# Optimization experiments

Measured on AMD Instinct MI355X. Metric: run time of the kernel, lower is better.

## Reference

```python
import jax, jax.numpy as jnp
import numpy as np

N = 100000      # nodes
E = 1600000     # edges (avg degree 16)
D = 128         # in_feats
C = 40          # n_classes
K = 4           # propagation steps
T = 2.0
DELTA = T / K   # 0.5
EPS = 1e-5      # LayerNorm eps


def setup_inputs() -> dict:
    key = jax.random.key(0)
    k1, k2, k3, k4, k5 = jax.random.split(key, 5)
    feat = jax.random.normal(k1, (N, D), jnp.float32)
    row = jax.random.randint(k2, (E,), 0, N, dtype=jnp.int32)
    col = jax.random.randint(k3, (E,), 0, N, dtype=jnp.int32)
    # fc: Linear(D -> C), xavier-ish scale
    W = jax.random.normal(k4, (C, D), jnp.float32) / np.sqrt(D)
    b = jax.random.normal(k5, (C,), jnp.float32) * 0.01
    # LayerNorm params
    gamma = jnp.ones((C,), jnp.float32)
    beta = jnp.zeros((C,), jnp.float32)
    return {"feat": feat, "row": row, "col": col, "W": W, "b": b,
            "gamma": gamma, "beta": beta}


def reference(feat, row, col, W, b, gamma, beta):
    # degrees of augmented adjacency A + I (row counts + self loop)
    deg = jnp.zeros((N,), feat.dtype).at[row].add(1.0) + 1.0
    dinv = jax.lax.rsqrt(deg)
    w_edge = dinv[row] * dinv[col]     # S[row,col] for off-diagonal entries
    w_self = dinv * dinv               # S[i,i] from the added self loop
    # h <- ((1-delta) I + delta S)^K @ feat, applied iteratively (same math as
    # precomputing the matrix power, but never materializes it)
    h = feat
    for _ in range(K):
        agg = jax.ops.segment_sum(h[col] * w_edge[:, None], row, num_segments=N)
        agg = agg + h * w_self[:, None]
        h = (1.0 - DELTA) * h + DELTA * agg
    # fc
    h = h @ W.T + b                    # [N, C]
    # LayerNorm over last dim
    mu = jnp.mean(h, axis=-1, keepdims=True)
    var = jnp.var(h, axis=-1, keepdims=True)
    h = (h - mu) * jax.lax.rsqrt(var + EPS) * gamma + beta
    return h
```

## Files before the change

kernel.cpp:

```cpp
#include <hip/hip_runtime.h>
#include <hip/hip_fp16.h>

#define N_NODES 100000
#define N_EDGES 1600000
#define D_FEAT  128
#define C_CLS   40
#define LN_EPS  1e-5f

#define RPB   256
#define NBKT  ((N_NODES + RPB - 1) / RPB)
#define BCAP  6144
#define TILE_E 4096
#define EBLK  ((N_EDGES + TILE_E - 1) / TILE_E)
#define NTILES (N_NODES / 16)
#define FCB   ((NTILES + 3) / 4)

#define ZPAD  8
#define QLO   ((N_NODES + ZPAD) * 4)
#define ZBYTES ((size_t)(N_NODES + ZPAD) * 80)

typedef __attribute__((ext_vector_type(8))) _Float16 half8;
typedef __attribute__((ext_vector_type(4))) float floatx4;
typedef __attribute__((ext_vector_type(4))) unsigned uintx4;

__device__ inline float2 h2f2(unsigned v) {
    __half2 h = *(__half2*)&v;
    return __half22float2(h);
}
__device__ inline unsigned f2h2(float x, float y) {
    __half2 h = __floats2half2_rn(x, y);
    return *(unsigned*)&h;
}

__global__ __launch_bounds__(256) void init_k(const float* __restrict__ W,
                                              _Float16* __restrict__ wh,
                                              int* __restrict__ bktsz,
                                              unsigned* __restrict__ z0,
                                              unsigned* __restrict__ z1) {
    int t = threadIdx.x;
    if (blockIdx.x < 20) {
        int i = blockIdx.x * 256 + t;
        if (i < C_CLS * D_FEAT) wh[i] = (_Float16)W[i];
        return;
    }
    for (int i = t; i < NBKT; i += 256) bktsz[i] = 0;
    if (t < 16) {
        z0[(size_t)N_NODES * 16 + t] = 0u;
        z1[(size_t)N_NODES * 16 + t] = 0u;
    }
    if (t < 4) {
        z0[(size_t)QLO * 4 + (size_t)N_NODES * 4 + t] = 0u;
        z1[(size_t)QLO * 4 + (size_t)N_NODES * 4 + t] = 0u;
    }
}

__global__ __launch_bounds__(256) void fcbin_k(const float* __restrict__ feat,
                                               const _Float16* __restrict__ wh,
                                               const int* __restrict__ row,
                                               const int* __restrict__ col,
                                               int* __restrict__ bktsz,
                                               int* __restrict__ csr_tmp,
                                               unsigned* __restrict__ z) {
    __shared__ int hist[NBKT];
    __shared__ int cbase[NBKT];
    __shared__ _Float16 zl[4][16][72];
    int t = threadIdx.x;
    if (blockIdx.x < EBLK) {
        int tile = blockIdx.x * TILE_E;
        for (int i = t; i < NBKT; i += 256) hist[i] = 0;
        __syncthreads();
        int r[16], c[16], pos[16];
        #pragma unroll
        for (int k = 0; k < 16; k++) {
            int e = tile + k * 256 + t;
            if (e < N_EDGES) {
                r[k] = row[e]; c[k] = col[e];
                pos[k] = atomicAdd(&hist[r[k] / RPB], 1);
            } else r[k] = -1;
        }
        __syncthreads();
        for (int i = t; i < NBKT; i += 256) {
            int h = hist[i];
            cbase[i] = h ? atomicAdd(&bktsz[i], h) : 0;
        }
        __syncthreads();
        #pragma unroll
        for (int k = 0; k < 16; k++) {
            if (r[k] >= 0) {
                int b = r[k] / RPB;
                int slot = cbase[b] + pos[k];
                if (slot < BCAP)
                    csr_tmp[b * BCAP + slot] = ((r[k] & (RPB - 1)) << 17) | c[k];
            }
        }
        return;
    }
    int wave = t >> 6, lane = t & 63;
    int m = lane & 15, quad = lane >> 4;
    int tile = (blockIdx.x - EBLK) * 4 + wave;
    bool valid = (tile < NTILES);
    int node0 = tile * 16;

    half8 bfrag[3][4];
    if (valid) {
        const half8* wh8 = (const half8*)wh;
        #pragma unroll
        for (int ct = 0; ct < 3; ct++) {
            int c = ct * 16 + m;
            bool ok = (c < C_CLS);
            #pragma unroll
            for (int ks = 0; ks < 4; ks++) {
                if (ok) {
                    bfrag[ct][ks] = wh8[c * 16 + ks * 4 + quad];
                } else {
                    #pragma unroll
                    for (int j = 0; j < 8; j++) bfrag[ct][ks][j] = (_Float16)0.0f;
                }
            }
        }
    }

    floatx4 acc0 = {0.f,0.f,0.f,0.f}, acc1 = acc0, acc2 = acc0;
    if (valid) {
        #pragma unroll
        for (int ks = 0; ks < 4; ks++) {
            const float4* ap = (const float4*)&feat[(node0 + m) * D_FEAT + ks * 32 + quad * 8];
            float4 a0 = ap[0], a1 = ap[1];
            half8 afrag;
            afrag[0] = (_Float16)a0.x; afrag[1] = (_Float16)a0.y;
            afrag[2] = (_Float16)a0.z; afrag[3] = (_Float16)a0.w;
            afrag[4] = (_Float16)a1.x; afrag[5] = (_Float16)a1.y;
            afrag[6] = (_Float16)a1.z; afrag[7] = (_Float16)a1.w;
            acc0 = __builtin_amdgcn_mfma_f32_16x16x32_f16(afrag, bfrag[0][ks], acc0, 0, 0, 0);
            acc1 = __builtin_amdgcn_mfma_f32_16x16x32_f16(afrag, bfrag[1][ks], acc1, 0, 0, 0);
            acc2 = __builtin_amdgcn_mfma_f32_16x16x32_f16(afrag, bfrag[2][ks], acc2, 0, 0, 0);
        }
    }

    if (valid) {
        #pragma unroll
        for (int r = 0; r < 4; r++) {
            int zrow = quad * 4 + r;
            zl[wave][zrow][m]      = (_Float16)acc0[r];
            zl[wave][zrow][16 + m] = (_Float16)acc1[r];
            zl[wave][zrow][32 + m] = (_Float16)acc2[r];
        }
    }
    __syncthreads();
    if (valid) {
        int zr = lane >> 2, part = lane & 3;
        uint4 lo = ((uint4*)&zl[wave][zr][0])[part];
        ((uint4*)z)[(size_t)(node0 + zr) * 4 + part] = lo;
        if (part == 0) {
            uint4 hi = *(uint4*)&zl[wave][zr][32];
            ((uint4*)z)[QLO + node0 + zr] = hi;
        }
    }
}

__global__ __launch_bounds__(256) void refine_k(const int* __restrict__ csr_tmp,
                                                const int* __restrict__ bktsz,
                                                int2* __restrict__ rowinfo,
                                                float2* __restrict__ rowc,
                                                int* __restrict__ csr_col,
                                                unsigned* __restrict__ z) {
    __shared__ int hist[RPB];
    __shared__ int psc[RPB];
    __shared__ int cur[RPB];
    __shared__ float dl[RPB];
    int b = blockIdx.x, t = threadIdx.x;
    int r0 = b * RPB;
    int nrows = min(RPB, N_NODES - r0);
    hist[t] = 0;
    __syncthreads();
    int cnt = bktsz[b];
    const int* base = csr_tmp + b * BCAP;
    for (int i = t; i < cnt; i += 256)
        atomicAdd(&hist[base[i] >> 17], 1);
    __syncthreads();
    int v = hist[t];
    psc[t] = v;
    __syncthreads();
    for (int off = 1; off < 256; off <<= 1) {
        int x = (t >= off) ? psc[t - off] : 0;
        __syncthreads();
        psc[t] += x;
        __syncthreads();
    }
    int start = b * BCAP + psc[t] - v;
    cur[t] = start;
    float fdeg = (float)v + 1.0f;
    float inv  = 1.0f / fdeg;
    dl[t] = rsqrtf(fdeg);
    if (t < nrows) {
        rowinfo[r0 + t] = make_int2(start, start + v);
        rowc[r0 + t]    = make_float2(0.5f + 0.5f * inv,
                                      0.5f * inv);
    }
    __syncthreads();
    for (int i = t; i < cnt; i += 256) {
        int pk = base[i];
        int lr = pk >> 17;
        int p = atomicAdd(&cur[lr], 1);
        csr_col[p] = pk & 0x1FFFF;
    }
    int totlo = nrows * 16;
    unsigned* zlo = z + (size_t)r0 * 16;
    for (int i = t; i < totlo; i += 256) {
        float s = dl[i >> 4];
        float2 f = h2f2(zlo[i]);
        zlo[i] = f2h2(f.x * s, f.y * s);
    }
    int tothi = nrows * 4;
    unsigned* zhi = z + (size_t)QLO * 4 + (size_t)r0 * 4;
    for (int i = t; i < tothi; i += 256) {
        float s = dl[i >> 2];
        float2 f = h2f2(zhi[i]);
        zhi[i] = f2h2(f.x * s, f.y * s);
    }
}

template<bool FINAL>
__global__ __launch_bounds__(256) void prop_u_t(const unsigned* __restrict__ hin,
                                                unsigned* __restrict__ hout,
                                                const int2* __restrict__ rowinfo,
                                                const float2* __restrict__ rowc,
                                                const int* __restrict__ csr_col,
                                                const float* __restrict__ bias,
                                                const float* __restrict__ gamma,
                                                const float* __restrict__ beta,
                                                float* __restrict__ out) {
    int t = threadIdx.x;
    int wave = t >> 6, lane = t & 63;
    int q   = lane >> 3;
    int sub = lane & 7;
    int node = blockIdx.x * 32 + wave * 8 + q;
    const uintx4* hin4 = (const uintx4*)hin;

    int mul  = (sub < 4) ? 4 : 1;
    int badd = (sub < 4) ? sub : QLO;

    uintx4 hv = hin4[(size_t)node * mul + badd];
    float2 rc = rowc[node];
    float acc[8] = {0.f,0.f,0.f,0.f,0.f,0.f,0.f,0.f};

    int2 ri = rowinfo[node];
    int j = ri.x, end = ri.y;
    int base = ri.x;

    int e[8];
    #pragma unroll
    for (int k = 0; k < 8; k++)
        e[k] = csr_col[(j + k < end) ? j + k : base];

    while (__any(j < end)) {
        uintx4 g[8];
        #pragma unroll
        for (int k = 0; k < 8; k++) {
            int c = (j + k < end) ? e[k] : N_NODES;
            g[k] = hin4[(size_t)c * mul + badd];
        }
        int j2 = j + 8;
        #pragma unroll
        for (int k = 0; k < 8; k++)
            e[k] = csr_col[(j2 + k < end) ? j2 + k : base];
        #pragma unroll
        for (int k = 0; k < 8; k++) {
            float2 f0 = h2f2(g[k].x), f1 = h2f2(g[k].y), f2 = h2f2(g[k].z), f3 = h2f2(g[k].w);
            acc[0] += f0.x; acc[1] += f0.y;
            acc[2] += f1.x; acc[3] += f1.y;
            acc[4] += f2.x; acc[5] += f2.y;
            acc[6] += f3.x; acc[7] += f3.y;
        }
        j = j2;
    }

    float2 h0 = h2f2(hv.x), h1 = h2f2(hv.y), h2 = h2f2(hv.z), h3 = h2f2(hv.w);
    float r8[8];
    r8[0] = rc.x * h0.x + rc.y * acc[0]; r8[1] = rc.x * h0.y + rc.y * acc[1];
    r8[2] = rc.x * h1.x + rc.y * acc[2]; r8[3] = rc.x * h1.y + rc.y * acc[3];
    r8[4] = rc.x * h2.x + rc.y * acc[4]; r8[5] = rc.x * h2.y + rc.y * acc[5];
    r8[6] = rc.x * h3.x + rc.y * acc[6]; r8[7] = rc.x * h3.y + rc.y * acc[7];

    if (!FINAL) {
        if (sub < 5) {
            uintx4 o;
            o.x = f2h2(r8[0], r8[1]);
            o.y = f2h2(r8[2], r8[3]);
            o.z = f2h2(r8[4], r8[5]);
            o.w = f2h2(r8[6], r8[7]);
            ((uintx4*)hout)[(size_t)node * mul + badd] = o;
        }
    } else {
        float fs = rsqrtf(2.0f * rc.x - 1.0f);
        bool realsub = (sub < 5);
        int cb = sub * 8;
        float vv[8];
        float s = 0.0f, ss = 0.0f;
        #pragma unroll
        for (int i = 0; i < 8; i++) {
            float x = realsub ? (fs * r8[i] + bias[cb + i]) : 0.0f;
            vv[i] = x;
            s += x; ss += x * x;
        }
        s  += __shfl_xor(s, 1);  s  += __shfl_xor(s, 2);  s  += __shfl_xor(s, 4);
        ss += __shfl_xor(ss, 1); ss += __shfl_xor(ss, 2); ss += __shfl_xor(ss, 4);
        float mean = s * (1.0f / C_CLS);
        float var  = ss * (1.0f / C_CLS) - mean * mean;
        float inv  = rsqrtf(var + LN_EPS);
        if (realsub) {
            float o8[8];
            #pragma unroll
            for (int i = 0; i < 8; i++)
                o8[i] = (vv[i] - mean) * inv * gamma[cb + i] + beta[cb + i];
            float* orow = out + (size_t)node * C_CLS + cb;
            ((float4*)orow)[0] = make_float4(o8[0], o8[1], o8[2], o8[3]);
            ((float4*)orow)[1] = make_float4(o8[4], o8[5], o8[6], o8[7]);
        }
    }
}

extern "C" void kernel_launch(void* const* d_in, const int* in_sizes, int n_in,
                              void* d_out, int out_size, void* d_ws, size_t ws_size,
                              hipStream_t stream) {
    const float* feat  = (const float*)d_in[0];
    const int*   row   = (const int*)d_in[1];
    const int*   col   = (const int*)d_in[2];
    const float* W     = (const float*)d_in[3];
    const float* b     = (const float*)d_in[4];
    const float* gamma = (const float*)d_in[5];
    const float* beta  = (const float*)d_in[6];
    float* out = (float*)d_out;

    char* ws = (char*)d_ws;
    size_t off = 0;
    auto alloc = [&](size_t bytes) {
        size_t o = off;
        off = (off + bytes + 255) & ~(size_t)255;
        return o;
    };
    float2*   rowc     = (float2*)  (ws + alloc((size_t)N_NODES * 8));
    int2*     rowinfo  = (int2*)    (ws + alloc((size_t)N_NODES * 8));
    int*      bktsz    = (int*)     (ws + alloc((size_t)NBKT * 4));
    _Float16* wh       = (_Float16*)(ws + alloc((size_t)C_CLS * D_FEAT * 2));
    int*      csr_tmp  = (int*)     (ws + alloc((size_t)NBKT * BCAP * 4));
    int*      csr_col  = (int*)     (ws + alloc((size_t)NBKT * BCAP * 4));
    unsigned* z0       = (unsigned*)(ws + alloc(ZBYTES));
    unsigned* z1       = (unsigned*)(ws + alloc(ZBYTES));

    init_k<<<21, 256, 0, stream>>>(W, wh, bktsz, z0, z1);
    fcbin_k<<<EBLK + FCB, 256, 0, stream>>>(feat, wh, row, col, bktsz, csr_tmp, z0);
    refine_k<<<NBKT, 256, 0, stream>>>(csr_tmp, bktsz, rowinfo, rowc, csr_col, z0);

    int pgrid = N_NODES / 32;
    prop_u_t<false><<<pgrid, 256, 0, stream>>>(z0, z1, rowinfo, rowc, csr_col,
                                               nullptr, nullptr, nullptr, nullptr);
    prop_u_t<false><<<pgrid, 256, 0, stream>>>(z1, z0, rowinfo, rowc, csr_col,
                                               nullptr, nullptr, nullptr, nullptr);
    prop_u_t<false><<<pgrid, 256, 0, stream>>>(z0, z1, rowinfo, rowc, csr_col,
                                               nullptr, nullptr, nullptr, nullptr);
    prop_u_t<true><<<pgrid, 256, 0, stream>>>(z1, nullptr, rowinfo, rowc, csr_col,
                                              b, gamma, beta, out);
}
```

Before: 268.9 us.

## Sort nodes by degree within buckets to balance propagation waves

The refine kernel now builds a per-bucket permutation of nodes ordered by in-degree, using an LDS histogram and a prefix scan, and writes it to a new perm array. Each propagation kernel maps its thread groups through this permutation, so nodes handled by the same wave have similar degrees and less lane divergence in the edge loop. Refine also caches bucket edges in LDS so the second pass does not reload them from global memory. In exchange, each propagation kernel pays an extra indirection load, and output and feature accesses become scattered within each 256-node bucket.

```diff
diff --git a/kernel.cpp b/kernel.cpp
--- a/kernel.cpp
+++ b/kernel.cpp
@@ -10,6 +10,7 @@
 #define RPB   256
 #define NBKT  ((N_NODES + RPB - 1) / RPB)
 #define BCAP  6144
+#define ECAP  5120
 #define TILE_E 4096
 #define EBLK  ((N_EDGES + TILE_E - 1) / TILE_E)
 #define NTILES (N_NODES / 16)
@@ -163,20 +164,28 @@
                                                 int2* __restrict__ rowinfo,
                                                 float2* __restrict__ rowc,
                                                 int* __restrict__ csr_col,
+                                                int* __restrict__ perm,
                                                 unsigned* __restrict__ z) {
-    __shared__ int hist[RPB];
-    __shared__ int psc[RPB];
-    __shared__ int cur[RPB];
+    __shared__ int   hist[RPB];
+    __shared__ int   psc[RPB];
+    __shared__ int   cur[RPB];
     __shared__ float dl[RPB];
+    __shared__ int   dh[RPB];
+    __shared__ int   dps[RPB];
+    __shared__ int   ecache[ECAP];
     int b = blockIdx.x, t = threadIdx.x;
     int r0 = b * RPB;
     int nrows = min(RPB, N_NODES - r0);
     hist[t] = 0;
+    dh[t] = 0;
     __syncthreads();
     int cnt = bktsz[b];
     const int* base = csr_tmp + b * BCAP;
-    for (int i = t; i < cnt; i += 256)
-        atomicAdd(&hist[base[i] >> 17], 1);
+    for (int i = t; i < cnt; i += 256) {
+        int pk = base[i];
+        if (i < ECAP) ecache[i] = pk;
+        atomicAdd(&hist[pk >> 17], 1);
+    }
     __syncthreads();
     int v = hist[t];
     psc[t] = v;
@@ -192,14 +201,28 @@
     float fdeg = (float)v + 1.0f;
     float inv  = 1.0f / fdeg;
     dl[t] = rsqrtf(fdeg);
+    int dcap = min(v, 255);
+    int drank = 0;
     if (t < nrows) {
         rowinfo[r0 + t] = make_int2(start, start + v);
         rowc[r0 + t]    = make_float2(0.5f + 0.5f * inv,
                                       0.5f * inv);
-    }
+        drank = atomicAdd(&dh[dcap], 1);
+    }
+    __syncthreads();
+    dps[t] = dh[t];
+    __syncthreads();
+    for (int off = 1; off < 256; off <<= 1) {
+        int x = (t >= off) ? dps[t - off] : 0;
+        __syncthreads();
+        dps[t] += x;
+        __syncthreads();
+    }
+    if (t < nrows)
+        perm[r0 + (dps[dcap] - dh[dcap]) + drank] = r0 + t;
     __syncthreads();
     for (int i = t; i < cnt; i += 256) {
-        int pk = base[i];
+        int pk = (i < ECAP) ? ecache[i] : base[i];
         int lr = pk >> 17;
         int p = atomicAdd(&cur[lr], 1);
         csr_col[p] = pk & 0x1FFFF;
@@ -226,6 +249,7 @@
                                                 const int2* __restrict__ rowinfo,
                                                 const float2* __restrict__ rowc,
                                                 const int* __restrict__ csr_col,
+                                                const int* __restrict__ perm,
                                                 const float* __restrict__ bias,
                                                 const float* __restrict__ gamma,
                                                 const float* __restrict__ beta,
@@ -234,7 +258,7 @@
     int wave = t >> 6, lane = t & 63;
     int q   = lane >> 3;
     int sub = lane & 7;
-    int node = blockIdx.x * 32 + wave * 8 + q;
+    int node = perm[blockIdx.x * 32 + wave * 8 + q];
     const uintx4* hin4 = (const uintx4*)hin;
 
     int mul  = (sub < 4) ? 4 : 1;
@@ -341,6 +365,7 @@
     };
     float2*   rowc     = (float2*)  (ws + alloc((size_t)N_NODES * 8));
     int2*     rowinfo  = (int2*)    (ws + alloc((size_t)N_NODES * 8));
+    int*      perm     = (int*)     (ws + alloc((size_t)N_NODES * 4));
     int*      bktsz    = (int*)     (ws + alloc((size_t)NBKT * 4));
     _Float16* wh       = (_Float16*)(ws + alloc((size_t)C_CLS * D_FEAT * 2));
     int*      csr_tmp  = (int*)     (ws + alloc((size_t)NBKT * BCAP * 4));
@@ -350,15 +375,15 @@
 
     init_k<<<21, 256, 0, stream>>>(W, wh, bktsz, z0, z1);
     fcbin_k<<<EBLK + FCB, 256, 0, stream>>>(feat, wh, row, col, bktsz, csr_tmp, z0);
-    refine_k<<<NBKT, 256, 0, stream>>>(csr_tmp, bktsz, rowinfo, rowc, csr_col, z0);
+    refine_k<<<NBKT, 256, 0, stream>>>(csr_tmp, bktsz, rowinfo, rowc, csr_col, perm, z0);
 
     int pgrid = N_NODES / 32;
-    prop_u_t<false><<<pgrid, 256, 0, stream>>>(z0, z1, rowinfo, rowc, csr_col,
+    prop_u_t<false><<<pgrid, 256, 0, stream>>>(z0, z1, rowinfo, rowc, csr_col, perm,
                                                nullptr, nullptr, nullptr, nullptr);
-    prop_u_t<false><<<pgrid, 256, 0, stream>>>(z1, z0, rowinfo, rowc, csr_col,
+    prop_u_t<false><<<pgrid, 256, 0, stream>>>(z1, z0, rowinfo, rowc, csr_col, perm,
                                                nullptr, nullptr, nullptr, nullptr);
-    prop_u_t<false><<<pgrid, 256, 0, stream>>>(z0, z1, rowinfo, rowc, csr_col,
+    prop_u_t<false><<<pgrid, 256, 0, stream>>>(z0, z1, rowinfo, rowc, csr_col, perm,
                                                nullptr, nullptr, nullptr, nullptr);
-    prop_u_t<true><<<pgrid, 256, 0, stream>>>(z1, nullptr, rowinfo, rowc, csr_col,
+    prop_u_t<true><<<pgrid, 256, 0, stream>>>(z1, nullptr, rowinfo, rowc, csr_col, perm,
                                               b, gamma, beta, out);
 }
```

Result: slower. 322.4 us (+19.9%).
